# Kernel optimization log

Measured on AMD Instinct MI355X. Metric: run time of the kernel, lower is better.

The kernel has to match this reference:

```python
import jax, jax.numpy as jnp
import numpy as np

N_NODES = 100000
N_EDGES = 1600000
IN_DIM, HID_DIM, OUT_DIM = 128, 64, 32
NEG_SLOPE = 0.2  # PyG GATConv default negative_slope


def gat_conv(x, src, dst, num_nodes, W, a_src, a_dst, bias):
    # x: [N, in], W: [in, out], a_src/a_dst: [out], bias: [out]
    h = x @ W                                        # [N, out]
    alpha_s = h @ a_src                              # [N] per-node source score
    alpha_d = h @ a_dst                              # [N] per-node target score
    e = jax.nn.leaky_relu(alpha_s[src] + alpha_d[dst], NEG_SLOPE)  # [E]
    # segment softmax over incoming edges of each dst node
    m = jax.ops.segment_max(e, dst, num_segments=num_nodes)        # [N]
    ex = jnp.exp(e - m[dst])                                        # [E]
    z = jax.ops.segment_sum(ex, dst, num_segments=num_nodes)        # [N]
    coef = ex / z[dst]                                              # [E]
    out = jax.ops.segment_sum(coef[:, None] * h[src], dst, num_segments=num_nodes)
    return out + bias


def setup_inputs() -> dict:
    key = jax.random.key(0)
    ks = jax.random.split(key, 10)
    x = jax.random.normal(ks[0], (N_NODES, IN_DIM), dtype=jnp.float32)
    edge_index = jax.random.randint(ks[1], (2, N_EDGES), 0, N_NODES, dtype=jnp.int64)
    s = 0.1
    W1 = jax.random.normal(ks[2], (IN_DIM, HID_DIM), dtype=jnp.float32) * s
    a_src1 = jax.random.normal(ks[3], (HID_DIM,), dtype=jnp.float32) * s
    a_dst1 = jax.random.normal(ks[4], (HID_DIM,), dtype=jnp.float32) * s
    b1 = jnp.zeros((HID_DIM,), dtype=jnp.float32)
    W2 = jax.random.normal(ks[5], (HID_DIM, OUT_DIM), dtype=jnp.float32) * s
    a_src2 = jax.random.normal(ks[6], (OUT_DIM,), dtype=jnp.float32) * s
    a_dst2 = jax.random.normal(ks[7], (OUT_DIM,), dtype=jnp.float32) * s
    b2 = jnp.zeros((OUT_DIM,), dtype=jnp.float32)
    return {"x": x, "edge_index": edge_index, "W1": W1, "a_src1": a_src1,
            "a_dst1": a_dst1, "b1": b1, "W2": W2, "a_src2": a_src2,
            "a_dst2": a_dst2, "b2": b2}


def reference(x, edge_index, W1, a_src1, a_dst1, b1, W2, a_src2, a_dst2, b2):
    n = x.shape[0]
    loops = jnp.arange(n, dtype=edge_index.dtype)
    src = jnp.concatenate([edge_index[0], loops])  # add_self_loops=True default
    dst = jnp.concatenate([edge_index[1], loops])
    h = jax.nn.relu(gat_conv(x, src, dst, n, W1, a_src1, a_dst1, b1))
    out = gat_conv(h, src, dst, n, W2, a_src2, a_dst2, b2)
    return jax.nn.log_softmax(out, axis=1)
```

## Files before the change

kernel.cpp:

```cpp
#include <hip/hip_runtime.h>

#define N_NODES 100000
#define N_EDGES 1600000
#define ET (N_EDGES + N_NODES)
#define NEG_SLOPE 0.2f

#define BSHIFT 9
#define BW 512
#define NBUCK ((N_NODES + BW - 1) / BW)
#define BCAP 10240
#define BINCH 2048

typedef unsigned short u16;
typedef unsigned int u32;

__device__ __forceinline__ float bf2f(u16 v) {
    return __uint_as_float(((u32)v) << 16);
}
__device__ __forceinline__ u16 f2bf(float f) {
    u32 u = __float_as_uint(f);
    u32 r = (u + 0x7FFFu + ((u >> 16) & 1u)) >> 16;
    return (u16)r;
}
__device__ __forceinline__ float lrelu(float x) { return x > 0.f ? x : NEG_SLOPE * x; }
__device__ __forceinline__ float ldf(const void* p, int i, int bf) {
    return bf ? bf2f(((const u16*)p)[i]) : ((const float*)p)[i];
}
__device__ __forceinline__ int get_dst(const int* __restrict__ ei, int e, int ei64) {
    if (e < N_EDGES) return ei64 ? ei[2 * (N_EDGES + e)] : ei[N_EDGES + e];
    return e - N_EDGES;
}
__device__ __forceinline__ int get_src(const int* __restrict__ ei, int e, int ei64) {
    if (e < N_EDGES) return ei64 ? ei[2 * e] : ei[e];
    return e - N_EDGES;
}

__device__ __forceinline__ void fma8(float wt, uint4 qv, float (&acc)[8]) {
    acc[0] = fmaf(wt, __uint_as_float(qv.x << 16), acc[0]);
    acc[1] = fmaf(wt, __uint_as_float(qv.x & 0xFFFF0000u), acc[1]);
    acc[2] = fmaf(wt, __uint_as_float(qv.y << 16), acc[2]);
    acc[3] = fmaf(wt, __uint_as_float(qv.y & 0xFFFF0000u), acc[3]);
    acc[4] = fmaf(wt, __uint_as_float(qv.z << 16), acc[4]);
    acc[5] = fmaf(wt, __uint_as_float(qv.z & 0xFFFF0000u), acc[5]);
    acc[6] = fmaf(wt, __uint_as_float(qv.w << 16), acc[6]);
    acc[7] = fmaf(wt, __uint_as_float(qv.w & 0xFFFF0000u), acc[7]);
}

__global__ void detect_kernel(const u32* __restrict__ x32, const int* __restrict__ ei,
                              int* __restrict__ flags, int* __restrict__ bcnt) {
    int lane = threadIdx.x;
    for (int i = lane; i < 256; i += 64) bcnt[i] = 0;
    u32 e = (x32[lane] >> 7) & 0xFFu;
    int ok = (e >= 96u && e <= 143u) ? 1 : 0;
    int cnt = (int)__popcll(__ballot(ok));
    int nz = (ei[2 * lane + 1] != 0) + (ei[2 * (lane + 64) + 1] != 0);
    #pragma unroll
    for (int off = 32; off > 0; off >>= 1) nz += __shfl_xor(nz, off);
    if (lane == 0) { flags[0] = (cnt >= 48) ? 1 : 0; flags[1] = (nz == 0) ? 1 : 0; }
}

__global__ __launch_bounds__(256) void bin_kernel(
    const int* __restrict__ ei, const int* __restrict__ flags,
    int* __restrict__ bcnt, u32* __restrict__ bbuf)
{
    __shared__ int hist[NBUCK];
    const int t = threadIdx.x;
    const int base = blockIdx.x * BINCH;
    const int ei64 = flags[1];
    for (int i = t; i < NBUCK; i += 256) hist[i] = 0;
    __syncthreads();

    int dloc[8], sloc[8];
    #pragma unroll
    for (int p = 0; p < 8; ++p) {
        int e = base + t + p * 256;
        if (e < ET) {
            dloc[p] = get_dst(ei, e, ei64);
            sloc[p] = get_src(ei, e, ei64);
            atomicAdd(&hist[dloc[p] >> BSHIFT], 1);
        } else {
            dloc[p] = -1; sloc[p] = 0;
        }
    }
    __syncthreads();
    for (int i = t; i < NBUCK; i += 256) {
        int c = hist[i];
        hist[i] = (c > 0) ? atomicAdd(&bcnt[i], c) : 0;
    }
    __syncthreads();
    #pragma unroll
    for (int p = 0; p < 8; ++p) {
        if (dloc[p] >= 0) {
            int b = dloc[p] >> BSHIFT;
            int pos = atomicAdd(&hist[b], 1);
            if (pos < BCAP)
                bbuf[(size_t)b * BCAP + pos] =
                    ((u32)(dloc[p] & (BW - 1)) << 17) | (u32)sloc[p];
        }
    }
}

__global__ __launch_bounds__(256) void bscan_kernel(
    const int* __restrict__ bcnt, int* __restrict__ bbase)
{
    __shared__ int sd[256];
    int t = threadIdx.x;
    int v = (t < NBUCK) ? min(bcnt[t], BCAP) : 0;
    sd[t] = v;
    __syncthreads();
    for (int off = 1; off < 256; off <<= 1) {
        int x = (t >= off) ? sd[t - off] : 0;
        __syncthreads();
        sd[t] += x;
        __syncthreads();
    }
    if (t < NBUCK) bbase[t] = sd[t] - v;
    if (t == NBUCK - 1) bbase[NBUCK] = sd[t];
}

__global__ __launch_bounds__(1024) void scatter_kernel(
    const int* __restrict__ bcnt, const int* __restrict__ bbase,
    const u32* __restrict__ bbuf, int* __restrict__ rowptr, int* __restrict__ ssrc)
{
    __shared__ int hist[BW];
    __shared__ int cur[BW];
    __shared__ int wtot[4];
    __shared__ int lds_s[BCAP];
    const int t = threadIdx.x;
    const int b = blockIdx.x;
    const int cnt = min(bcnt[b], BCAP);
    const int base = bbase[b];
    const u32* mybuf = bbuf + (size_t)b * BCAP;

    if (t < BW) hist[t] = 0;
    __syncthreads();
    for (int i = t; i < cnt; i += 1024) atomicAdd(&hist[(int)(mybuf[i] >> 17)], 1);
    __syncthreads();
    int a0 = 0, a1 = 0, s = 0, v = 0;
    const int lane = t & 63, wid = t >> 6;
    if (t < 256) {
        a0 = hist[2 * t]; a1 = hist[2 * t + 1];
        s = a0 + a1;
        v = s;
        #pragma unroll
        for (int off = 1; off < 64; off <<= 1) {
            int n = __shfl_up(v, off);
            if (lane >= off) v += n;
        }
        if (lane == 63) wtot[wid] = v;
    }
    __syncthreads();
    if (t == 0) {
        int acc = 0;
        #pragma unroll
        for (int w = 0; w < 4; ++w) { int tmp = wtot[w]; wtot[w] = acc; acc += tmp; }
    }
    __syncthreads();
    if (t < 256) {
        int excl = v + wtot[wid] - s;
        cur[2 * t] = excl;
        cur[2 * t + 1] = excl + a0;
    }
    __syncthreads();
    if (t < BW) {
        int g = b * BW + t;
        if (g < N_NODES) rowptr[g] = base + cur[t];
    }
    if (b == NBUCK - 1 && t == 0) rowptr[N_NODES] = bbase[NBUCK];
    __syncthreads();
    for (int i = t; i < cnt; i += 1024) {
        u32 code = mybuf[i];
        int pos = atomicAdd(&cur[(int)(code >> 17)], 1);
        lds_s[pos] = (int)(code & 0x1FFFFu);
    }
    __syncthreads();
    for (int i = t; i < cnt; i += 1024) ssrc[base + i] = lds_s[i];
}

__global__ __launch_bounds__(256) void gemm1_kernel(
    const float* __restrict__ x, const float* __restrict__ W,
    const void* __restrict__ a_src, const void* __restrict__ a_dst,
    const int* __restrict__ flags,
    u16* __restrict__ h, float* __restrict__ as_, float* __restrict__ ad_)
{
    __shared__ float xs[256 * 33];
    __shared__ float Wl[32 * 64];
    const int t = threadIdx.x;
    const int node0 = blockIdx.x * 256;
    const int bf = flags[0];
    const int ng = t >> 3;
    const int cg = t & 7;

    float acc[8][8];
    #pragma unroll
    for (int i = 0; i < 8; ++i)
        #pragma unroll
        for (int j = 0; j < 8; ++j) acc[i][j] = 0.f;

    for (int kc = 0; kc < 4; ++kc) {
        const int kb = kc * 32;
        const int c4 = t & 7;
        #pragma unroll
        for (int p = 0; p < 8; ++p) {
            int row = (t >> 3) + p * 32;
            int n = node0 + row;
            float4 vv = make_float4(0.f, 0.f, 0.f, 0.f);
            if (n < N_NODES) {
                if (!bf) {
                    vv = *(const float4*)(x + (size_t)n * 128 + kb + c4 * 4);
                } else {
                    const u16* xh = (const u16*)x;
                    vv.x = bf2f(xh[(size_t)n * 128 + kb + c4 * 4 + 0]);
                    vv.y = bf2f(xh[(size_t)n * 128 + kb + c4 * 4 + 1]);
                    vv.z = bf2f(xh[(size_t)n * 128 + kb + c4 * 4 + 2]);
                    vv.w = bf2f(xh[(size_t)n * 128 + kb + c4 * 4 + 3]);
                }
            }
            float* dstp = &xs[row * 33 + c4 * 4];
            dstp[0] = vv.x; dstp[1] = vv.y; dstp[2] = vv.z; dstp[3] = vv.w;
        }
        if (!bf) {
            #pragma unroll
            for (int qq = 0; qq < 2; ++qq) {
                int f4 = t * 2 + qq;
                ((float4*)Wl)[f4] = ((const float4*)(W + (size_t)kb * 64))[f4];
            }
        } else {
            const u16* Wh = (const u16*)W;
            for (int i = t; i < 2048; i += 256) Wl[i] = bf2f(Wh[(size_t)kb * 64 + i]);
        }
        __syncthreads();

        for (int kk = 0; kk < 32; ++kk) {
            float xr[8];
            #pragma unroll
            for (int i = 0; i < 8; ++i) xr[i] = xs[(ng * 8 + i) * 33 + kk];
            float4 w0 = *(const float4*)&Wl[kk * 64 + cg * 8];
            float4 w1 = *(const float4*)&Wl[kk * 64 + cg * 8 + 4];
            const float wr[8] = {w0.x, w0.y, w0.z, w0.w, w1.x, w1.y, w1.z, w1.w};
            #pragma unroll
            for (int i = 0; i < 8; ++i)
                #pragma unroll
                for (int j = 0; j < 8; ++j)
                    acc[i][j] = fmaf(xr[i], wr[j], acc[i][j]);
        }
        __syncthreads();
    }

    float av[8], dv[8];
    #pragma unroll
    for (int j = 0; j < 8; ++j) {
        av[j] = ldf(a_src, cg * 8 + j, bf);
        dv[j] = ldf(a_dst, cg * 8 + j, bf);
    }
    #pragma unroll
    for (int i = 0; i < 8; ++i) {
        int n = node0 + ng * 8 + i;
        float ps = 0.f, pd = 0.f;
        #pragma unroll
        for (int j = 0; j < 8; ++j) { ps += acc[i][j] * av[j]; pd += acc[i][j] * dv[j]; }
        #pragma unroll
        for (int off = 1; off < 8; off <<= 1) {
            ps += __shfl_xor(ps, off);
            pd += __shfl_xor(pd, off);
        }
        if (n < N_NODES) {
            uint4 hv;
            hv.x = (u32)f2bf(acc[i][0]) | ((u32)f2bf(acc[i][1]) << 16);
            hv.y = (u32)f2bf(acc[i][2]) | ((u32)f2bf(acc[i][3]) << 16);
            hv.z = (u32)f2bf(acc[i][4]) | ((u32)f2bf(acc[i][5]) << 16);
            hv.w = (u32)f2bf(acc[i][6]) | ((u32)f2bf(acc[i][7]) << 16);
            *(uint4*)&h[(size_t)n * 64 + cg * 8] = hv;
            if (cg == 0) { as_[n] = ps; ad_[n] = pd; }
        }
    }
}

template<int SH>
__global__ __launch_bounds__(256) void score_kernel(
    const int* __restrict__ rowptr, const int* __restrict__ ssrc,
    const float* __restrict__ as_, const float* __restrict__ ad_,
    uint2* __restrict__ wexs)
{
    const int lane = threadIdx.x & 63;
    const int dst = blockIdx.x * 4 + (threadIdx.x >> 6);
    if (dst >= N_NODES) return;
    const int beg = rowptr[dst], end = rowptr[dst + 1];
    const int deg = end - beg;
    const float add = ad_[dst];

    if (deg <= 64) {
        int j = beg + lane;
        bool valid = j < end;
        int sj = valid ? ssrc[j] : 0;
        float sc = valid ? lrelu(as_[sj] + add) : -1e30f;
        float m = sc;
        #pragma unroll
        for (int off = 32; off > 0; off >>= 1) m = fmaxf(m, __shfl_xor(m, off));
        float ex = __expf(sc - m);
        float l = ex;
        #pragma unroll
        for (int off = 32; off > 0; off >>= 1) l += __shfl_xor(l, off);
        if (valid)
            wexs[j] = make_uint2(__float_as_uint(ex / l), ((u32)sj) << SH);
    } else {
        float m = -1e30f, l = 0.f;
        for (int base = beg; base < end; base += 64) {
            int j = base + lane;
            bool valid = j < end;
            float sc = valid ? lrelu(as_[ssrc[j]] + add) : -1e30f;
            float cm = sc;
            #pragma unroll
            for (int off = 32; off > 0; off >>= 1) cm = fmaxf(cm, __shfl_xor(cm, off));
            float nm = fmaxf(m, cm);
            float cs = __expf(sc - nm);
            #pragma unroll
            for (int off = 32; off > 0; off >>= 1) cs += __shfl_xor(cs, off);
            l = l * __expf(m - nm) + cs;
            m = nm;
        }
        float inv = 1.f / l;
        for (int base = beg; base < end; base += 64) {
            int j = base + lane;
            if (j < end) {
                int sj = ssrc[j];
                wexs[j] = make_uint2(
                    __float_as_uint(__expf(lrelu(as_[sj] + add) - m) * inv),
                    ((u32)sj) << SH);
            }
        }
    }
}

__global__ __launch_bounds__(256) void gather64_g2_kernel(
    const int* __restrict__ rowptr, const uint2* __restrict__ wexs,
    const u16* __restrict__ h, const void* __restrict__ b1,
    const u32* __restrict__ W32, const void* __restrict__ a_src,
    const void* __restrict__ a_dst, const int* __restrict__ flags,
    u16* __restrict__ h2, float* __restrict__ as2, float* __restrict__ ad2)
{
    __shared__ float W2t[32 * 66];
    __shared__ float hin_lds[8 * 64];
    const int tid = threadIdx.x;
    const int hl = tid & 31;
    const int dreal = blockIdx.x * 8 + (tid >> 5);
    const int dst = min(dreal, N_NODES - 1);
    const int bf = flags[0];

    if (bf) {
        for (int i = tid; i < 1024; i += 256) {
            u32 u = W32[i];
            int k = i >> 4;
            int c = (2 * i) & 31;
            W2t[c * 66 + k] = __uint_as_float(u << 16);
            W2t[(c + 1) * 66 + k] = __uint_as_float(u & 0xFFFF0000u);
        }
    } else {
        for (int i = tid; i < 2048; i += 256) {
            int k = i >> 5, c = i & 31;
            W2t[c * 66 + k] = __uint_as_float(W32[i]);
        }
    }
    __syncthreads();

    const int beg = rowptr[dst];
    const int deg = rowptr[dst + 1] - beg;
    const int e4 = hl >> 3;
    const int i8 = hl & 7;
    const char* __restrict__ hb = (const char*)h;
    const u32 boff = (u32)(i8 * 16);

    float acc[8] = {0.f, 0.f, 0.f, 0.f, 0.f, 0.f, 0.f, 0.f};

    #pragma unroll
    for (int g = 0; g < 8; ++g) {
        int eidx = g * 4 + e4;
        bool valid = eidx < deg;
        uint2 p = wexs[beg + (valid ? eidx : 0)];
        float w = valid ? __uint_as_float(p.x) : 0.f;
        uint4 qv = *(const uint4*)(hb + (size_t)(p.y + boff));
        fma8(w, qv, acc);
    }
    int mdeg = max(deg, __shfl_xor(deg, 32));
    for (int g = 8; g * 4 < mdeg; ++g) {
        int eidx = g * 4 + e4;
        bool valid = eidx < deg;
        uint2 p = wexs[beg + (valid ? eidx : 0)];
        float w = valid ? __uint_as_float(p.x) : 0.f;
        uint4 qv = *(const uint4*)(hb + (size_t)(p.y + boff));
        fma8(w, qv, acc);
    }

    #pragma unroll
    for (int c = 0; c < 8; ++c) {
        acc[c] += __shfl_xor(acc[c], 8);
        acc[c] += __shfl_xor(acc[c], 16);
    }

    float* hin_s = &hin_lds[(tid >> 5) * 64];
    if (hl < 8) {
        float4 v0, v1;
        v0.x = fmaxf(acc[0] + ldf(b1, hl * 8 + 0, bf), 0.f);
        v0.y = fmaxf(acc[1] + ldf(b1, hl * 8 + 1, bf), 0.f);
        v0.z = fmaxf(acc[2] + ldf(b1, hl * 8 + 2, bf), 0.f);
        v0.w = fmaxf(acc[3] + ldf(b1, hl * 8 + 3, bf), 0.f);
        v1.x = fmaxf(acc[4] + ldf(b1, hl * 8 + 4, bf), 0.f);
        v1.y = fmaxf(acc[5] + ldf(b1, hl * 8 + 5, bf), 0.f);
        v1.z = fmaxf(acc[6] + ldf(b1, hl * 8 + 6, bf), 0.f);
        v1.w = fmaxf(acc[7] + ldf(b1, hl * 8 + 7, bf), 0.f);
        *(float4*)&hin_s[hl * 8] = v0;
        *(float4*)&hin_s[hl * 8 + 4] = v1;
    }
    __builtin_amdgcn_wave_barrier();
    asm volatile("s_waitcnt lgkmcnt(0)" ::: "memory");

    float o = 0.f;
    #pragma unroll 8
    for (int k = 0; k < 64; k += 2) {
        float2 hv = *(const float2*)&hin_s[k];
        float2 wv = *(const float2*)&W2t[hl * 66 + k];
        o = fmaf(hv.x, wv.x, o);
        o = fmaf(hv.y, wv.y, o);
    }

    float ps = o * ldf(a_src, hl, bf);
    float pd = o * ldf(a_dst, hl, bf);
    #pragma unroll
    for (int off = 1; off < 32; off <<= 1) {
        ps += __shfl_xor(ps, off);
        pd += __shfl_xor(pd, off);
    }
    u32 hbits = (u32)f2bf(o);
    u32 other = (u32)__shfl_xor((int)hbits, 1);
    if (dreal < N_NODES) {
        if ((hl & 1) == 0)
            *((u32*)h2 + (size_t)dst * 16 + (hl >> 1)) = hbits | (other << 16);
        if (hl == 0) { as2[dst] = ps; ad2[dst] = pd; }
    }
    __builtin_amdgcn_wave_barrier();
}

__global__ __launch_bounds__(256) void gather32_lsm_kernel(
    const int* __restrict__ rowptr, const uint2* __restrict__ wexs,
    const u16* __restrict__ h, const void* __restrict__ b2,
    const int* __restrict__ flags, float* __restrict__ out)
{
    const int tid = threadIdx.x;
    const int hl = tid & 31;
    const int dreal = blockIdx.x * 8 + (tid >> 5);
    const int dst = min(dreal, N_NODES - 1);
    const int beg = rowptr[dst];
    const int deg = rowptr[dst + 1] - beg;
    const int e8 = hl >> 2;
    const int i4 = hl & 3;
    const int bf = flags[0];
    const char* __restrict__ hb = (const char*)h;
    const u32 boff = (u32)(i4 * 16);

    float acc[8] = {0.f, 0.f, 0.f, 0.f, 0.f, 0.f, 0.f, 0.f};

    #pragma unroll
    for (int g = 0; g < 4; ++g) {
        int eidx = g * 8 + e8;
        bool valid = eidx < deg;
        uint2 p = wexs[beg + (valid ? eidx : 0)];
        float w = valid ? __uint_as_float(p.x) : 0.f;
        uint4 qv = *(const uint4*)(hb + (size_t)(p.y + boff));
        fma8(w, qv, acc);
    }
    int mdeg = max(deg, __shfl_xor(deg, 32));
    for (int g = 4; g * 8 < mdeg; ++g) {
        int eidx = g * 8 + e8;
        bool valid = eidx < deg;
        uint2 p = wexs[beg + (valid ? eidx : 0)];
        float w = valid ? __uint_as_float(p.x) : 0.f;
        uint4 qv = *(const uint4*)(hb + (size_t)(p.y + boff));
        fma8(w, qv, acc);
    }

    #pragma unroll
    for (int c = 0; c < 8; ++c) {
        acc[c] += __shfl_xor(acc[c], 4);
        acc[c] += __shfl_xor(acc[c], 8);
        acc[c] += __shfl_xor(acc[c], 16);
    }

    float v[8];
    #pragma unroll
    for (int c = 0; c < 8; ++c) v[c] = acc[c] + ldf(b2, i4 * 8 + c, bf);
    float mx = v[0];
    #pragma unroll
    for (int c = 1; c < 8; ++c) mx = fmaxf(mx, v[c]);
    mx = fmaxf(mx, __shfl_xor(mx, 1));
    mx = fmaxf(mx, __shfl_xor(mx, 2));
    float ss = 0.f;
    #pragma unroll
    for (int c = 0; c < 8; ++c) ss += __expf(v[c] - mx);
    ss += __shfl_xor(ss, 1);
    ss += __shfl_xor(ss, 2);
    float lg = mx + __logf(ss);
    if (e8 == 0 && dreal < N_NODES) {
        *(float4*)&out[(size_t)dst * 32 + i4 * 8] =
            make_float4(v[0] - lg, v[1] - lg, v[2] - lg, v[3] - lg);
        *(float4*)&out[(size_t)dst * 32 + i4 * 8 + 4] =
            make_float4(v[4] - lg, v[5] - lg, v[6] - lg, v[7] - lg);
    }
}

extern "C" void kernel_launch(void* const* d_in, const int* in_sizes, int n_in,
                              void* d_out, int out_size, void* d_ws, size_t ws_size,
                              hipStream_t stream) {
    const float* x   = (const float*)d_in[0];
    const int* ei    = (const int*)d_in[1];
    const float* W1  = (const float*)d_in[2];
    const void* a_s1 = d_in[3];
    const void* a_d1 = d_in[4];
    const void* b1   = d_in[5];
    const u32* W2    = (const u32*)d_in[6];
    const void* a_s2 = d_in[7];
    const void* a_d2 = d_in[8];
    const void* b2   = d_in[9];
    float* out = (float*)d_out;

    char* base = (char*)d_ws;
    int* flags = (int*)base;
    u16* h     = (u16*)(base + 64);
    char* q = base + 64 + (size_t)N_NODES * 64 * 2;
    float* as1 = (float*)q; q += (size_t)N_NODES * 4;
    float* ad1 = (float*)q; q += (size_t)N_NODES * 4;
    float* as2 = (float*)q; q += (size_t)N_NODES * 4;
    float* ad2 = (float*)q; q += (size_t)N_NODES * 4;
    u16* h2    = (u16*)q;   q += (size_t)N_NODES * 64 * 4;
    int* rowptr = (int*)q;  q += (size_t)(N_NODES + 16) * 4;
    int* ssrc   = (int*)q;  q += (size_t)ET * 4;
    int* bcnt   = (int*)q;  q += 256 * 4;
    int* bbase  = (int*)q;  q += 256 * 4;
    q = (char*)(((size_t)q + 255) & ~(size_t)255);
    u32*  bbuf  = (u32*)q;
    uint2* wexs = (uint2*)q;

    detect_kernel<<<1, 64, 0, stream>>>((const u32*)x, ei, flags, bcnt);

    bin_kernel<<<(ET + BINCH - 1) / BINCH, 256, 0, stream>>>(ei, flags, bcnt, bbuf);
    bscan_kernel<<<1, 256, 0, stream>>>(bcnt, bbase);
    scatter_kernel<<<NBUCK, 1024, 0, stream>>>(bcnt, bbase, bbuf, rowptr, ssrc);

    gemm1_kernel<<<(N_NODES + 255) / 256, 256, 0, stream>>>(x, W1, a_s1, a_d1, flags, h, as1, ad1);
    score_kernel<7><<<(N_NODES + 3) / 4, 256, 0, stream>>>(rowptr, ssrc, as1, ad1, wexs);
    gather64_g2_kernel<<<(N_NODES + 7) / 8, 256, 0, stream>>>(
        rowptr, wexs, h, b1, W2, a_s2, a_d2, flags, h2, as2, ad2);

    score_kernel<6><<<(N_NODES + 3) / 4, 256, 0, stream>>>(rowptr, ssrc, as2, ad2, wexs);
    gather32_lsm_kernel<<<(N_NODES + 7) / 8, 256, 0, stream>>>(rowptr, wexs, h2, b2, flags, out);
}
```

Measured before the change: 331.5 us.

## Fuse edge softmax scoring into gather kernels and drop wexs buffer

Removes the separate score kernels and computes each destination's segment softmax inside the gather kernels, with one 32-lane half-wave per destination. Source row offsets and coefficients are broadcast via shuffles, so the edge-weight buffer is never written and read back. The layer-2 weight matrix is kept in LDS row-major instead of padded transposed, and the h2 workspace is resized. High-degree nodes now take a two-pass path that reloads ssrc and as_, and degrees between 33 and 64 move off the single-pass fast path.

```diff
diff --git a/kernel.cpp b/kernel.cpp
--- a/kernel.cpp
+++ b/kernel.cpp
@@ -276,73 +276,19 @@
     }
 }
 
-template<int SH>
-__global__ __launch_bounds__(256) void score_kernel(
+__global__ __launch_bounds__(256) void gather64_g2_kernel(
     const int* __restrict__ rowptr, const int* __restrict__ ssrc,
     const float* __restrict__ as_, const float* __restrict__ ad_,
-    uint2* __restrict__ wexs)
-{
-    const int lane = threadIdx.x & 63;
-    const int dst = blockIdx.x * 4 + (threadIdx.x >> 6);
-    if (dst >= N_NODES) return;
-    const int beg = rowptr[dst], end = rowptr[dst + 1];
-    const int deg = end - beg;
-    const float add = ad_[dst];
-
-    if (deg <= 64) {
-        int j = beg + lane;
-        bool valid = j < end;
-        int sj = valid ? ssrc[j] : 0;
-        float sc = valid ? lrelu(as_[sj] + add) : -1e30f;
-        float m = sc;
-        #pragma unroll
-        for (int off = 32; off > 0; off >>= 1) m = fmaxf(m, __shfl_xor(m, off));
-        float ex = __expf(sc - m);
-        float l = ex;
-        #pragma unroll
-        for (int off = 32; off > 0; off >>= 1) l += __shfl_xor(l, off);
-        if (valid)
-            wexs[j] = make_uint2(__float_as_uint(ex / l), ((u32)sj) << SH);
-    } else {
-        float m = -1e30f, l = 0.f;
-        for (int base = beg; base < end; base += 64) {
-            int j = base + lane;
-            bool valid = j < end;
-            float sc = valid ? lrelu(as_[ssrc[j]] + add) : -1e30f;
-            float cm = sc;
-            #pragma unroll
-            for (int off = 32; off > 0; off >>= 1) cm = fmaxf(cm, __shfl_xor(cm, off));
-            float nm = fmaxf(m, cm);
-            float cs = __expf(sc - nm);
-            #pragma unroll
-            for (int off = 32; off > 0; off >>= 1) cs += __shfl_xor(cs, off);
-            l = l * __expf(m - nm) + cs;
-            m = nm;
-        }
-        float inv = 1.f / l;
-        for (int base = beg; base < end; base += 64) {
-            int j = base + lane;
-            if (j < end) {
-                int sj = ssrc[j];
-                wexs[j] = make_uint2(
-                    __float_as_uint(__expf(lrelu(as_[sj] + add) - m) * inv),
-                    ((u32)sj) << SH);
-            }
-        }
-    }
-}
-
-__global__ __launch_bounds__(256) void gather64_g2_kernel(
-    const int* __restrict__ rowptr, const uint2* __restrict__ wexs,
     const u16* __restrict__ h, const void* __restrict__ b1,
-    const u32* __restrict__ W32, const void* __restrict__ a_src,
-    const void* __restrict__ a_dst, const int* __restrict__ flags,
+    const u32* __restrict__ W32, const void* __restrict__ a_src2,
+    const void* __restrict__ a_dst2, const int* __restrict__ flags,
     u16* __restrict__ h2, float* __restrict__ as2, float* __restrict__ ad2)
 {
-    __shared__ float W2t[32 * 66];
+    __shared__ float W2s[64 * 32];
     __shared__ float hin_lds[8 * 64];
     const int tid = threadIdx.x;
     const int hl = tid & 31;
+    const int hbase = tid & 32;
     const int dreal = blockIdx.x * 8 + (tid >> 5);
     const int dst = min(dreal, N_NODES - 1);
     const int bf = flags[0];
@@ -350,21 +296,18 @@
     if (bf) {
         for (int i = tid; i < 1024; i += 256) {
             u32 u = W32[i];
-            int k = i >> 4;
-            int c = (2 * i) & 31;
-            W2t[c * 66 + k] = __uint_as_float(u << 16);
-            W2t[(c + 1) * 66 + k] = __uint_as_float(u & 0xFFFF0000u);
+            *(float2*)&W2s[2 * i] = make_float2(__uint_as_float(u << 16),
+                                                __uint_as_float(u & 0xFFFF0000u));
         }
     } else {
-        for (int i = tid; i < 2048; i += 256) {
-            int k = i >> 5, c = i & 31;
-            W2t[c * 66 + k] = __uint_as_float(W32[i]);
-        }
+        for (int i = tid; i < 2048; i += 256) W2s[i] = __uint_as_float(W32[i]);
     }
     __syncthreads();
 
     const int beg = rowptr[dst];
-    const int deg = rowptr[dst + 1] - beg;
+    const int end = rowptr[dst + 1];
+    const int deg = end - beg;
+    const float add = ad_[dst];
     const int e4 = hl >> 3;
     const int i8 = hl & 7;
     const char* __restrict__ hb = (const char*)h;
@@ -372,23 +315,72 @@
 
     float acc[8] = {0.f, 0.f, 0.f, 0.f, 0.f, 0.f, 0.f, 0.f};
 
-    #pragma unroll
-    for (int g = 0; g < 8; ++g) {
-        int eidx = g * 4 + e4;
-        bool valid = eidx < deg;
-        uint2 p = wexs[beg + (valid ? eidx : 0)];
-        float w = valid ? __uint_as_float(p.x) : 0.f;
-        uint4 qv = *(const uint4*)(hb + (size_t)(p.y + boff));
-        fma8(w, qv, acc);
-    }
-    int mdeg = max(deg, __shfl_xor(deg, 32));
-    for (int g = 8; g * 4 < mdeg; ++g) {
-        int eidx = g * 4 + e4;
-        bool valid = eidx < deg;
-        uint2 p = wexs[beg + (valid ? eidx : 0)];
-        float w = valid ? __uint_as_float(p.x) : 0.f;
-        uint4 qv = *(const uint4*)(hb + (size_t)(p.y + boff));
-        fma8(w, qv, acc);
+    if (deg <= 32) {
+        int j = beg + hl;
+        bool valid = hl < deg;
+        int sj = valid ? ssrc[j] : 0;
+        float asv = as_[sj];
+        int rowoff = sj << 7;
+        int ga[8];
+        #pragma unroll
+        for (int g = 0; g < 8; ++g) ga[g] = __shfl(rowoff, hbase + g * 4 + e4);
+        uint4 q[8];
+        #pragma unroll
+        for (int g = 0; g < 8; ++g)
+            q[g] = *(const uint4*)(hb + (size_t)((u32)ga[g] + boff));
+
+        float sc = valid ? lrelu(asv + add) : -1e30f;
+        float m = sc;
+        #pragma unroll
+        for (int off = 16; off > 0; off >>= 1) m = fmaxf(m, __shfl_xor(m, off));
+        float ex = __expf(sc - m);
+        float l = ex;
+        #pragma unroll
+        for (int off = 16; off > 0; off >>= 1) l += __shfl_xor(l, off);
+        float coef = ex / l;
+
+        float w[8];
+        #pragma unroll
+        for (int g = 0; g < 8; ++g) w[g] = __shfl(coef, hbase + g * 4 + e4);
+        #pragma unroll
+        for (int g = 0; g < 8; ++g) fma8(w[g], q[g], acc);
+    } else {
+        float m = -1e30f, l = 0.f;
+        for (int base = beg; base < end; base += 32) {
+            int j = base + hl;
+            bool valid = j < end;
+            float sc = valid ? lrelu(as_[ssrc[j]] + add) : -1e30f;
+            float cm = sc;
+            #pragma unroll
+            for (int off = 16; off > 0; off >>= 1) cm = fmaxf(cm, __shfl_xor(cm, off));
+            float nm = fmaxf(m, cm);
+            float cs = __expf(sc - nm);
+            #pragma unroll
+            for (int off = 16; off > 0; off >>= 1) cs += __shfl_xor(cs, off);
+            l = l * __expf(m - nm) + cs;
+            m = nm;
+        }
+        float inv = 1.f / l;
+        for (int base = beg; base < end; base += 32) {
+            int j = base + hl;
+            bool valid = j < end;
+            int sj = valid ? ssrc[j] : 0;
+            int rowoff = sj << 7;
+            int ga[8];
+            #pragma unroll
+            for (int g = 0; g < 8; ++g) ga[g] = __shfl(rowoff, hbase + g * 4 + e4);
+            uint4 q[8];
+            #pragma unroll
+            for (int g = 0; g < 8; ++g)
+                q[g] = *(const uint4*)(hb + (size_t)((u32)ga[g] + boff));
+            float sc = valid ? lrelu(as_[sj] + add) : -1e30f;
+            float coef = __expf(sc - m) * inv;
+            float w[8];
+            #pragma unroll
+            for (int g = 0; g < 8; ++g) w[g] = __shfl(coef, hbase + g * 4 + e4);
+            #pragma unroll
+            for (int g = 0; g < 8; ++g) fma8(w[g], q[g], acc);
+        }
     }
 
     #pragma unroll
@@ -415,16 +407,17 @@
     asm volatile("s_waitcnt lgkmcnt(0)" ::: "memory");
 
     float o = 0.f;
-    #pragma unroll 8
-    for (int k = 0; k < 64; k += 2) {
-        float2 hv = *(const float2*)&hin_s[k];
-        float2 wv = *(const float2*)&W2t[hl * 66 + k];
-        o = fmaf(hv.x, wv.x, o);
-        o = fmaf(hv.y, wv.y, o);
-    }
-
-    float ps = o * ldf(a_src, hl, bf);
-    float pd = o * ldf(a_dst, hl, bf);
+    #pragma unroll 16
+    for (int k = 0; k < 64; k += 4) {
+        float4 hv = *(const float4*)&hin_s[k];
+        o = fmaf(hv.x, W2s[(k + 0) * 32 + hl], o);
+        o = fmaf(hv.y, W2s[(k + 1) * 32 + hl], o);
+        o = fmaf(hv.z, W2s[(k + 2) * 32 + hl], o);
+        o = fmaf(hv.w, W2s[(k + 3) * 32 + hl], o);
+    }
+
+    float ps = o * ldf(a_src2, hl, bf);
+    float pd = o * ldf(a_dst2, hl, bf);
     #pragma unroll
     for (int off = 1; off < 32; off <<= 1) {
         ps += __shfl_xor(ps, off);
@@ -441,16 +434,20 @@
 }
 
 __global__ __launch_bounds__(256) void gather32_lsm_kernel(
-    const int* __restrict__ rowptr, const uint2* __restrict__ wexs,
+    const int* __restrict__ rowptr, const int* __restrict__ ssrc,
+    const float* __restrict__ as_, const float* __restrict__ ad_,
     const u16* __restrict__ h, const void* __restrict__ b2,
     const int* __restrict__ flags, float* __restrict__ out)
 {
     const int tid = threadIdx.x;
     const int hl = tid & 31;
+    const int hbase = tid & 32;
     const int dreal = blockIdx.x * 8 + (tid >> 5);
     const int dst = min(dreal, N_NODES - 1);
     const int beg = rowptr[dst];
-    const int deg = rowptr[dst + 1] - beg;
+    const int end = rowptr[dst + 1];
+    const int deg = end - beg;
+    const float add = ad_[dst];
     const int e8 = hl >> 2;
     const int i4 = hl & 3;
     const int bf = flags[0];
@@ -459,23 +456,72 @@
 
     float acc[8] = {0.f, 0.f, 0.f, 0.f, 0.f, 0.f, 0.f, 0.f};
 
-    #pragma unroll
-    for (int g = 0; g < 4; ++g) {
-        int eidx = g * 8 + e8;
-        bool valid = eidx < deg;
-        uint2 p = wexs[beg + (valid ? eidx : 0)];
-        float w = valid ? __uint_as_float(p.x) : 0.f;
-        uint4 qv = *(const uint4*)(hb + (size_t)(p.y + boff));
-        fma8(w, qv, acc);
-    }
-    int mdeg = max(deg, __shfl_xor(deg, 32));
-    for (int g = 4; g * 8 < mdeg; ++g) {
-        int eidx = g * 8 + e8;
-        bool valid = eidx < deg;
-        uint2 p = wexs[beg + (valid ? eidx : 0)];
-        float w = valid ? __uint_as_float(p.x) : 0.f;
-        uint4 qv = *(const uint4*)(hb + (size_t)(p.y + boff));
-        fma8(w, qv, acc);
+    if (deg <= 32) {
+        int j = beg + hl;
+        bool valid = hl < deg;
+        int sj = valid ? ssrc[j] : 0;
+        float asv = as_[sj];
+        int rowoff = sj << 6;
+        int ga[4];
+        #pragma unroll
+        for (int g = 0; g < 4; ++g) ga[g] = __shfl(rowoff, hbase + g * 8 + e8);
+        uint4 q[4];
+        #pragma unroll
+        for (int g = 0; g < 4; ++g)
+            q[g] = *(const uint4*)(hb + (size_t)((u32)ga[g] + boff));
+
+        float sc = valid ? lrelu(asv + add) : -1e30f;
+        float m = sc;
+        #pragma unroll
+        for (int off = 16; off > 0; off >>= 1) m = fmaxf(m, __shfl_xor(m, off));
+        float ex = __expf(sc - m);
+        float l = ex;
+        #pragma unroll
+        for (int off = 16; off > 0; off >>= 1) l += __shfl_xor(l, off);
+        float coef = ex / l;
+
+        float w[4];
+        #pragma unroll
+        for (int g = 0; g < 4; ++g) w[g] = __shfl(coef, hbase + g * 8 + e8);
+        #pragma unroll
+        for (int g = 0; g < 4; ++g) fma8(w[g], q[g], acc);
+    } else {
+        float m = -1e30f, l = 0.f;
+        for (int base = beg; base < end; base += 32) {
+            int j = base + hl;
+            bool valid = j < end;
+            float sc = valid ? lrelu(as_[ssrc[j]] + add) : -1e30f;
+            float cm = sc;
+            #pragma unroll
+            for (int off = 16; off > 0; off >>= 1) cm = fmaxf(cm, __shfl_xor(cm, off));
+            float nm = fmaxf(m, cm);
+            float cs = __expf(sc - nm);
+            #pragma unroll
+            for (int off = 16; off > 0; off >>= 1) cs += __shfl_xor(cs, off);
+            l = l * __expf(m - nm) + cs;
+            m = nm;
+        }
+        float inv = 1.f / l;
+        for (int base = beg; base < end; base += 32) {
+            int j = base + hl;
+            bool valid = j < end;
+            int sj = valid ? ssrc[j] : 0;
+            int rowoff = sj << 6;
+            int ga[4];
+            #pragma unroll
+            for (int g = 0; g < 4; ++g) ga[g] = __shfl(rowoff, hbase + g * 8 + e8);
+            uint4 q[4];
+            #pragma unroll
+            for (int g = 0; g < 4; ++g)
+                q[g] = *(const uint4*)(hb + (size_t)((u32)ga[g] + boff));
+            float sc = valid ? lrelu(as_[sj] + add) : -1e30f;
+            float coef = __expf(sc - m) * inv;
+            float w[4];
+            #pragma unroll
+            for (int g = 0; g < 4; ++g) w[g] = __shfl(coef, hbase + g * 8 + e8);
+            #pragma unroll
+            for (int g = 0; g < 4; ++g) fma8(w[g], q[g], acc);
+        }
     }
 
     #pragma unroll
@@ -530,14 +576,13 @@
     float* ad1 = (float*)q; q += (size_t)N_NODES * 4;
     float* as2 = (float*)q; q += (size_t)N_NODES * 4;
     float* ad2 = (float*)q; q += (size_t)N_NODES * 4;
-    u16* h2    = (u16*)q;   q += (size_t)N_NODES * 64 * 4;
+    u16* h2    = (u16*)q;   q += (size_t)N_NODES * 32 * 2;
     int* rowptr = (int*)q;  q += (size_t)(N_NODES + 16) * 4;
     int* ssrc   = (int*)q;  q += (size_t)ET * 4;
     int* bcnt   = (int*)q;  q += 256 * 4;
     int* bbase  = (int*)q;  q += 256 * 4;
     q = (char*)(((size_t)q + 255) & ~(size_t)255);
     u32*  bbuf  = (u32*)q;
-    uint2* wexs = (uint2*)q;
 
     detect_kernel<<<1, 64, 0, stream>>>((const u32*)x, ei, flags, bcnt);
 
@@ -546,10 +591,9 @@
     scatter_kernel<<<NBUCK, 1024, 0, stream>>>(bcnt, bbase, bbuf, rowptr, ssrc);
 
     gemm1_kernel<<<(N_NODES + 255) / 256, 256, 0, stream>>>(x, W1, a_s1, a_d1, flags, h, as1, ad1);
-    score_kernel<7><<<(N_NODES + 3) / 4, 256, 0, stream>>>(rowptr, ssrc, as1, ad1, wexs);
     gather64_g2_kernel<<<(N_NODES + 7) / 8, 256, 0, stream>>>(
-        rowptr, wexs, h, b1, W2, a_s2, a_d2, flags, h2, as2, ad2);
-
-    score_kernel<6><<<(N_NODES + 3) / 4, 256, 0, stream>>>(rowptr, ssrc, as2, ad2, wexs);
-    gather32_lsm_kernel<<<(N_NODES + 7) / 8, 256, 0, stream>>>(rowptr, wexs, h2, b2, flags, out);
-}
+        rowptr, ssrc, as1, ad1, h, b1, W2, a_s2, a_d2, flags, h2, as2, ad2);
+
+    gather32_lsm_kernel<<<(N_NODES + 7) / 8, 256, 0, stream>>>(
+        rowptr, ssrc, as2, ad2, h2, b2, flags, out);
+}
```

Measured after the change: 301.9 us. -8.9%, faster.

## Fuse layer-2 attention scoring into final gather and re-lay W2 in LDS

Applied to the files above, without the earlier changes.

Drops the separate layer-2 score kernel and its per-edge weight buffer. The final gather kernel now reads source indices and per-node scores directly, computes unnormalised exponentials per edge and shares them across the half-wave with shuffles. It normalises the aggregate by the summed exponentials at the end. This removes one launch and a full write and re-read of per-edge weights and indices. The softmax skips the max subtraction, which risks overflow if scores get large. Separately, W2 is kept row-major in LDS so each thread reads a column with float4 broadcasts of the hidden vector.

```diff
diff --git a/kernel.cpp b/kernel.cpp
--- a/kernel.cpp
+++ b/kernel.cpp
@@ -276,8 +276,7 @@
     }
 }
 
-template<int SH>
-__global__ __launch_bounds__(256) void score_kernel(
+__global__ __launch_bounds__(256) void score1_kernel(
     const int* __restrict__ rowptr, const int* __restrict__ ssrc,
     const float* __restrict__ as_, const float* __restrict__ ad_,
     uint2* __restrict__ wexs)
@@ -302,7 +301,7 @@
         #pragma unroll
         for (int off = 32; off > 0; off >>= 1) l += __shfl_xor(l, off);
         if (valid)
-            wexs[j] = make_uint2(__float_as_uint(ex / l), ((u32)sj) << SH);
+            wexs[j] = make_uint2(__float_as_uint(ex / l), ((u32)sj) << 7);
     } else {
         float m = -1e30f, l = 0.f;
         for (int base = beg; base < end; base += 64) {
@@ -326,7 +325,7 @@
                 int sj = ssrc[j];
                 wexs[j] = make_uint2(
                     __float_as_uint(__expf(lrelu(as_[sj] + add) - m) * inv),
-                    ((u32)sj) << SH);
+                    ((u32)sj) << 7);
             }
         }
     }
@@ -335,11 +334,11 @@
 __global__ __launch_bounds__(256) void gather64_g2_kernel(
     const int* __restrict__ rowptr, const uint2* __restrict__ wexs,
     const u16* __restrict__ h, const void* __restrict__ b1,
-    const u32* __restrict__ W32, const void* __restrict__ a_src,
-    const void* __restrict__ a_dst, const int* __restrict__ flags,
+    const u32* __restrict__ W32, const void* __restrict__ a_src2,
+    const void* __restrict__ a_dst2, const int* __restrict__ flags,
     u16* __restrict__ h2, float* __restrict__ as2, float* __restrict__ ad2)
 {
-    __shared__ float W2t[32 * 66];
+    __shared__ float W2s[64 * 32];
     __shared__ float hin_lds[8 * 64];
     const int tid = threadIdx.x;
     const int hl = tid & 31;
@@ -350,16 +349,11 @@
     if (bf) {
         for (int i = tid; i < 1024; i += 256) {
             u32 u = W32[i];
-            int k = i >> 4;
-            int c = (2 * i) & 31;
-            W2t[c * 66 + k] = __uint_as_float(u << 16);
-            W2t[(c + 1) * 66 + k] = __uint_as_float(u & 0xFFFF0000u);
+            *(float2*)&W2s[2 * i] = make_float2(__uint_as_float(u << 16),
+                                                __uint_as_float(u & 0xFFFF0000u));
         }
     } else {
-        for (int i = tid; i < 2048; i += 256) {
-            int k = i >> 5, c = i & 31;
-            W2t[c * 66 + k] = __uint_as_float(W32[i]);
-        }
+        for (int i = tid; i < 2048; i += 256) W2s[i] = __uint_as_float(W32[i]);
     }
     __syncthreads();
 
@@ -415,16 +409,17 @@
     asm volatile("s_waitcnt lgkmcnt(0)" ::: "memory");
 
     float o = 0.f;
-    #pragma unroll 8
-    for (int k = 0; k < 64; k += 2) {
-        float2 hv = *(const float2*)&hin_s[k];
-        float2 wv = *(const float2*)&W2t[hl * 66 + k];
-        o = fmaf(hv.x, wv.x, o);
-        o = fmaf(hv.y, wv.y, o);
-    }
-
-    float ps = o * ldf(a_src, hl, bf);
-    float pd = o * ldf(a_dst, hl, bf);
+    #pragma unroll 16
+    for (int k = 0; k < 64; k += 4) {
+        float4 hv = *(const float4*)&hin_s[k];
+        o = fmaf(hv.x, W2s[(k + 0) * 32 + hl], o);
+        o = fmaf(hv.y, W2s[(k + 1) * 32 + hl], o);
+        o = fmaf(hv.z, W2s[(k + 2) * 32 + hl], o);
+        o = fmaf(hv.w, W2s[(k + 3) * 32 + hl], o);
+    }
+
+    float ps = o * ldf(a_src2, hl, bf);
+    float pd = o * ldf(a_dst2, hl, bf);
     #pragma unroll
     for (int off = 1; off < 32; off <<= 1) {
         ps += __shfl_xor(ps, off);
@@ -441,16 +436,19 @@
 }
 
 __global__ __launch_bounds__(256) void gather32_lsm_kernel(
-    const int* __restrict__ rowptr, const uint2* __restrict__ wexs,
+    const int* __restrict__ rowptr, const int* __restrict__ ssrc,
+    const float* __restrict__ as_, const float* __restrict__ ad_,
     const u16* __restrict__ h, const void* __restrict__ b2,
     const int* __restrict__ flags, float* __restrict__ out)
 {
     const int tid = threadIdx.x;
     const int hl = tid & 31;
+    const int hbase = tid & 32;
     const int dreal = blockIdx.x * 8 + (tid >> 5);
     const int dst = min(dreal, N_NODES - 1);
     const int beg = rowptr[dst];
-    const int deg = rowptr[dst + 1] - beg;
+    const int end = rowptr[dst + 1];
+    const float add = ad_[dst];
     const int e8 = hl >> 2;
     const int i4 = hl & 3;
     const int bf = flags[0];
@@ -458,25 +456,45 @@
     const u32 boff = (u32)(i4 * 16);
 
     float acc[8] = {0.f, 0.f, 0.f, 0.f, 0.f, 0.f, 0.f, 0.f};
-
-    #pragma unroll
-    for (int g = 0; g < 4; ++g) {
-        int eidx = g * 8 + e8;
-        bool valid = eidx < deg;
-        uint2 p = wexs[beg + (valid ? eidx : 0)];
-        float w = valid ? __uint_as_float(p.x) : 0.f;
-        uint4 qv = *(const uint4*)(hb + (size_t)(p.y + boff));
-        fma8(w, qv, acc);
-    }
-    int mdeg = max(deg, __shfl_xor(deg, 32));
-    for (int g = 4; g * 8 < mdeg; ++g) {
-        int eidx = g * 8 + e8;
-        bool valid = eidx < deg;
-        uint2 p = wexs[beg + (valid ? eidx : 0)];
-        float w = valid ? __uint_as_float(p.x) : 0.f;
-        uint4 qv = *(const uint4*)(hb + (size_t)(p.y + boff));
-        fma8(w, qv, acc);
-    }
+    float lacc = 0.f;
+
+    for (int eb = beg; eb < end; eb += 32) {
+        int j = eb + hl;
+        bool valid = j < end;
+        int sj = valid ? ssrc[j] : 0;
+        float asv = as_[sj];
+        int rowoff = sj << 6;
+        float sc = valid ? lrelu(asv + add) : -1e30f;
+        float ex = __expf(sc);
+        lacc += ex;
+
+        {
+            int l0 = hbase + e8;
+            int l1 = hbase + 8 + e8;
+            int ga0 = __shfl(rowoff, l0);
+            int ga1 = __shfl(rowoff, l1);
+            uint4 q0 = *(const uint4*)(hb + (size_t)((u32)ga0 + boff));
+            uint4 q1 = *(const uint4*)(hb + (size_t)((u32)ga1 + boff));
+            float w0 = __shfl(ex, l0);
+            float w1 = __shfl(ex, l1);
+            fma8(w0, q0, acc); fma8(w1, q1, acc);
+        }
+        if (end - eb > 16) {
+            int l2 = hbase + 16 + e8;
+            int l3 = hbase + 24 + e8;
+            int ga2 = __shfl(rowoff, l2);
+            int ga3 = __shfl(rowoff, l3);
+            uint4 q2 = *(const uint4*)(hb + (size_t)((u32)ga2 + boff));
+            uint4 q3 = *(const uint4*)(hb + (size_t)((u32)ga3 + boff));
+            float w2 = __shfl(ex, l2);
+            float w3 = __shfl(ex, l3);
+            fma8(w2, q2, acc); fma8(w3, q3, acc);
+        }
+    }
+
+    #pragma unroll
+    for (int off = 16; off > 0; off >>= 1) lacc += __shfl_xor(lacc, off);
+    float invl = 1.f / lacc;
 
     #pragma unroll
     for (int c = 0; c < 8; ++c) {
@@ -487,7 +505,7 @@
 
     float v[8];
     #pragma unroll
-    for (int c = 0; c < 8; ++c) v[c] = acc[c] + ldf(b2, i4 * 8 + c, bf);
+    for (int c = 0; c < 8; ++c) v[c] = fmaf(acc[c], invl, ldf(b2, i4 * 8 + c, bf));
     float mx = v[0];
     #pragma unroll
     for (int c = 1; c < 8; ++c) mx = fmaxf(mx, v[c]);
@@ -530,7 +548,7 @@
     float* ad1 = (float*)q; q += (size_t)N_NODES * 4;
     float* as2 = (float*)q; q += (size_t)N_NODES * 4;
     float* ad2 = (float*)q; q += (size_t)N_NODES * 4;
-    u16* h2    = (u16*)q;   q += (size_t)N_NODES * 64 * 4;
+    u16* h2    = (u16*)q;   q += (size_t)N_NODES * 32 * 2;
     int* rowptr = (int*)q;  q += (size_t)(N_NODES + 16) * 4;
     int* ssrc   = (int*)q;  q += (size_t)ET * 4;
     int* bcnt   = (int*)q;  q += 256 * 4;
@@ -546,10 +564,10 @@
     scatter_kernel<<<NBUCK, 1024, 0, stream>>>(bcnt, bbase, bbuf, rowptr, ssrc);
 
     gemm1_kernel<<<(N_NODES + 255) / 256, 256, 0, stream>>>(x, W1, a_s1, a_d1, flags, h, as1, ad1);
-    score_kernel<7><<<(N_NODES + 3) / 4, 256, 0, stream>>>(rowptr, ssrc, as1, ad1, wexs);
+    score1_kernel<<<(N_NODES + 3) / 4, 256, 0, stream>>>(rowptr, ssrc, as1, ad1, wexs);
     gather64_g2_kernel<<<(N_NODES + 7) / 8, 256, 0, stream>>>(
         rowptr, wexs, h, b1, W2, a_s2, a_d2, flags, h2, as2, ad2);
 
-    score_kernel<6><<<(N_NODES + 3) / 4, 256, 0, stream>>>(rowptr, ssrc, as2, ad2, wexs);
-    gather32_lsm_kernel<<<(N_NODES + 7) / 8, 256, 0, stream>>>(rowptr, wexs, h2, b2, flags, out);
-}
+    gather32_lsm_kernel<<<(N_NODES + 7) / 8, 256, 0, stream>>>(
+        rowptr, ssrc, as2, ad2, h2, b2, flags, out);
+}
```

Result: slower. 345.5 us (+4.2%).
